# Kernel optimization log

Measured on AMD Instinct MI355X. Metric: run time of the kernel, lower is better.

## Reference

```python
import jax, jax.numpy as jnp
import numpy as np

B, C, N, T = 8, 32, 4000, 12
KT = 3
TS = 6          # tem_size
SUP_ORD_CH = (2 * 3 + 1) * C  # (order*support_len+1)*c_in = 224
EPS = 1e-5


def setup_inputs() -> dict:
    key = jax.random.key(0)
    ks = jax.random.split(key, 20)
    inp = {
        "x": jax.random.normal(ks[0], (B, C, N, T), dtype=jnp.float32),
        # dense normalized supports (scaled uniform, like row-normalized adjacency)
        "A0": jax.random.uniform(ks[1], (N, N), dtype=jnp.float32) / N,
        "A1": jax.random.uniform(ks[2], (N, N), dtype=jnp.float32) / N,
        "A2": jax.random.uniform(ks[3], (N, N), dtype=jnp.float32) / N,
        # conv1: 1x1 Conv2d(32 -> 32), bias
        "conv1_w": jax.random.normal(ks[4], (C, C), dtype=jnp.float32) * 0.05,
        "conv1_b": jnp.zeros((C,), dtype=jnp.float32),
        # multigcn mlp: Conv2d(224 -> 64, kernel (1, Kt)), bias
        "mlp_w": jax.random.normal(ks[5], (2 * C, SUP_ORD_CH, 1, KT), dtype=jnp.float32) * 0.02,
        "mlp_b": jnp.zeros((2 * C,), dtype=jnp.float32),
        # conv_temp1: 1x1 Conv2d over time axis (10 -> 6), bias
        "ct1_w": jax.random.normal(ks[6], (TS, T - KT + 1), dtype=jnp.float32) * 0.1,
        "ct1_b": jnp.zeros((TS,), dtype=jnp.float32),
        # TATT_1 params
        "tat_c1_w": jax.random.normal(ks[7], (C,), dtype=jnp.float32) * 0.1,   # Conv2d(c_in->1,1x1,no bias)
        "tat_c2_w": jax.random.normal(ks[8], (N,), dtype=jnp.float32) * 0.01,  # Conv2d(N->1,1x1,no bias)
        "tat_w": jax.random.normal(ks[9], (N, C), dtype=jnp.float32) * 0.01,
        "tat_bias": jnp.zeros((TS, TS), dtype=jnp.float32),
        "tat_v": jax.random.normal(ks[10], (TS, TS), dtype=jnp.float32) * 0.3,
        "bn1_g": jnp.ones((TS,), dtype=jnp.float32),
        "bn1_b": jnp.zeros((TS,), dtype=jnp.float32),
        # final BatchNorm2d(c_out)
        "bn2_g": jnp.ones((C,), dtype=jnp.float32),
        "bn2_b": jnp.zeros((C,), dtype=jnp.float32),
    }
    return inp


def reference(x, A0, A1, A2, conv1_w, conv1_b, mlp_w, mlp_b, ct1_w, ct1_b,
              tat_c1_w, tat_c2_w, tat_w, tat_bias, tat_v, bn1_g, bn1_b,
              bn2_g, bn2_b):
    # residual = conv1(x)  (1x1 conv over channels)
    residual = jnp.einsum('oc,bcnl->bonl', conv1_w, x) + conv1_b[None, :, None, None]

    # multi_gcn_time: nconv does A<-A.T then einsum('ncvl,vw->ncwl'),
    # i.e. out[..,w,..] = sum_v x[..,v,..] * A[w,v]
    outs = [x]
    for A in (A0, A1, A2):
        x1 = jnp.einsum('bcvl,wv->bcwl', x, A)
        outs.append(x1)
        x2 = jnp.einsum('bcvl,wv->bcwl', x1, A)
        outs.append(x2)
    h = jnp.concatenate(outs, axis=1)  # (B, 224, N, T)
    h = jax.lax.conv_general_dilated(
        h, mlp_w, window_strides=(1, 1), padding='VALID',
        dimension_numbers=('NCHW', 'OIHW', 'NCHW')) + mlp_b[None, :, None, None]  # (B,64,N,10)

    # gated tanh * sigmoid
    x1, x2 = jnp.split(h, 2, axis=1)
    g = jnp.tanh(x1) * jax.nn.sigmoid(x2)  # (B,32,N,10)

    # conv_temp1: 1x1 conv over the TIME axis (10 -> 6)
    g = jnp.einsum('ql,bcnl->bcnq', ct1_w, g) + ct1_b[None, None, None, :]  # (B,32,N,6)

    # TATT_1 temporal attention coefficients
    f1 = jnp.einsum('c,bcnt->btn', tat_c1_w, g)                       # (B,6,N)
    f2 = jnp.einsum('n,bcnt->bct', tat_c2_w, g)                       # (B,32,6)
    logits = jax.nn.sigmoid(jnp.einsum('btn,nc,bcs->bts', f1, tat_w, f2) + tat_bias)
    logits = jnp.einsum('ts,bsq->btq', tat_v, logits)                 # (B,6,6)
    # BatchNorm1d(tem_size) applied after permute(0,2,1): channel = q axis
    lp = jnp.transpose(logits, (0, 2, 1))
    mu = lp.mean(axis=(0, 2), keepdims=True)
    var = lp.var(axis=(0, 2), keepdims=True)
    lp = (lp - mu) / jnp.sqrt(var + EPS) * bn1_g[None, :, None] + bn1_b[None, :, None]
    logits = jnp.transpose(lp, (0, 2, 1))
    coefs = jax.nn.softmax(logits, axis=-1)                           # (B,6,6)

    # x = einsum('bcnl,blq->bcnq', x, T_coef.transpose(-1,-2))
    Tc = jnp.transpose(coefs, (0, 2, 1))
    out = jnp.einsum('bcnl,blq->bcnq', g, Tc)                         # (B,32,N,6)

    y = out + residual[:, :, :, -out.shape[3]:]
    # BatchNorm2d(c_out), training-mode batch stats
    mu2 = y.mean(axis=(0, 2, 3), keepdims=True)
    var2 = y.var(axis=(0, 2, 3), keepdims=True)
    return (y - mu2) / jnp.sqrt(var2 + EPS) * bn2_g[None, :, None, None] + bn2_b[None, :, None, None]
```

## Files before the change

### kernel.cpp

```cpp
#include <hip/hip_runtime.h>
#include <hip/hip_bf16.h>
#include <cstdint>
#include <cstddef>


typedef __attribute__((ext_vector_type(8))) short s16x8;
typedef __attribute__((ext_vector_type(4))) short s16x4;
typedef __attribute__((ext_vector_type(4))) float f32x4;

#define DEVFN __device__ __forceinline__

DEVFN void gload16(const void* g, void* l) {
  __builtin_amdgcn_global_load_lds((const __attribute__((address_space(1))) unsigned int*)g,
                                   (__attribute__((address_space(3))) unsigned int*)l, 16, 0, 0);
}

DEVFN unsigned short f2bf(float f) {
  union { float f; unsigned int u; } v; v.f = f;
  unsigned int u = v.u;
  return (unsigned short)((u + 0x7fffu + ((u >> 16) & 1u)) >> 16);
}

__global__ void k_transpose(const float* __restrict__ x,
                            unsigned short* __restrict__ Xt,
                            unsigned short* __restrict__ Scat) {
  __shared__ float ldsT[32 * 417];
  int v0 = blockIdx.x * 32;
  int b = blockIdx.y;
  int tid = threadIdx.x;
  for (int i = tid; i < 1024; i += 256) {
    int c = i >> 5, vv = i & 31;
    const float* src = x + ((size_t)(b * 32 + c) * 4000 + v0 + vv) * 12;
    f32x4 a0 = *(const f32x4*)(src);
    f32x4 a1 = *(const f32x4*)(src + 4);
    f32x4 a2 = *(const f32x4*)(src + 8);
    float* d = ldsT + c * 417 + vv * 13;
    d[0] = a0.x; d[1] = a0.y; d[2] = a0.z; d[3] = a0.w;
    d[4] = a1.x; d[5] = a1.y; d[6] = a1.z; d[7] = a1.w;
    d[8] = a2.x; d[9] = a2.y; d[10] = a2.z; d[11] = a2.w;
  }
  __syncthreads();
  for (int unit = tid; unit < 384; unit += 256) {
    int l = unit >> 5, c = unit & 31;
    alignas(16) unsigned short tmp[32];
#pragma unroll
    for (int vv = 0; vv < 32; ++vv) tmp[vv] = f2bf(ldsT[c * 417 + vv * 13 + l]);
    unsigned short* dst = Xt + (size_t)(b * 384 + l * 32 + c) * 4096 + v0;
#pragma unroll
    for (int j = 0; j < 4; ++j) *(s16x8*)(dst + j * 8) = *(const s16x8*)(tmp + j * 8);
  }
  for (int unit = tid; unit < 384; unit += 256) {
    int l = unit >> 5, vv = unit & 31;
    alignas(16) unsigned short tmp[32];
#pragma unroll
    for (int c = 0; c < 32; ++c) tmp[c] = f2bf(ldsT[c * 417 + vv * 13 + l]);
    int bn = b * 4000 + v0 + vv;
    unsigned short* dst = Scat + ((((size_t)l * 500 + (bn >> 6)) * 28) * 64 + (bn & 63)) * 8;
#pragma unroll
    for (int j = 0; j < 4; ++j) *(s16x8*)(dst + j * 512) = *(const s16x8*)(tmp + j * 8);
  }
}

__global__ void k_castA(const float* __restrict__ A, unsigned short* __restrict__ Abf) {
  int idx = blockIdx.x * 256 + threadIdx.x;
  int r = idx >> 10;
  int c4 = (idx & 1023) << 2;
  alignas(8) unsigned short o[4] = {0, 0, 0, 0};
  if (r < 4000 && c4 < 4000) {
    f32x4 v = *(const f32x4*)(A + (size_t)r * 4000 + c4);
    o[0] = f2bf(v.x); o[1] = f2bf(v.y); o[2] = f2bf(v.z); o[3] = f2bf(v.w);
  }
  *(s16x4*)(Abf + (size_t)r * 4096 + c4) = *(const s16x4*)o;
}

__global__ void k_wcat(const float* __restrict__ mlp_w, unsigned short* __restrict__ Wcat) {
  int i = blockIdx.x * 256 + threadIdx.x;
  if (i >= 43008) return;
  int e = i & 7;
  int j = (i >> 3) % 21;
  int rs = (i >> 3) / 21;
  int s = rs & 1, row = rs >> 1;
  int kt = j / 7, ks = j % 7;
  int p2 = row >> 6, g = (row >> 4) & 3, lr = row & 15;
  int oc = (s ? 32 : 0) + p2 * 16 + lr;
  int ic = ks * 32 + g * 8 + e;
  Wcat[i] = f2bf(mlp_w[((size_t)oc * 224 + ic) * 3 + kt]);
}

#define MFMA_(a, b, c) __builtin_amdgcn_mfma_f32_16x16x32_bf16(a, b, c, 0, 0, 0)

#define STGA3(ab, t) do {                                                        \
    const unsigned short* _s = aSrc + (size_t)(t) * 64;                          \
    unsigned short* _l = smem + (ab) * 12288;                                    \
    gload16(_s,          _l + tid * 8);                                          \
    gload16(_s + 262144, _l + (512 + tid) * 8);                                  \
    gload16(_s + 524288, _l + (1024 + tid) * 8);                                 \
  } while (0)

#define STGB3(pr, h, t) do {                                                     \
    const unsigned short* _s = bSrc + (size_t)(h) * 524288 + (size_t)(t) * 64;   \
    unsigned short* _l = smem + 36864 + ((pr) * 2 + (h)) * 8192;                 \
    gload16(_s,          _l + tid * 8);                                          \
    gload16(_s + 262144, _l + (512 + tid) * 8);                                  \
  } while (0)

#define LDA3(ab, f, kk) (*(const s16x8*)(smem + (ab) * 12288 + aoff + (f) * 1024 + ((kk) ? sxor : 0)))
#define LDB3(pr, nf, kk) (*(const s16x8*)(smem + 36864 + ((pr) * 2 + hb) * 8192 + boff + (nf) * 1024 + ((kk) ? sxor : 0)))

#define PHASE3(ab, pr, mp, FIRST, STAGE_CODE, VM) do {                           \
    s16x8 a00 = LDA3(ab, 2 * (mp), 0),     a01 = LDA3(ab, 2 * (mp), 1);          \
    s16x8 a10 = LDA3(ab, 2 * (mp) + 1, 0), a11 = LDA3(ab, 2 * (mp) + 1, 1);      \
    if (FIRST) {                                                                 \
      _Pragma("unroll")                                                          \
      for (int nf = 0; nf < 4; ++nf) { bfr[nf][0] = LDB3(pr, nf, 0); bfr[nf][1] = LDB3(pr, nf, 1); } \
    }                                                                            \
    STAGE_CODE;                                                                  \
    if ((VM) == 1)      asm volatile("s_waitcnt vmcnt(5)" ::: "memory");         \
    else if ((VM) == 2) asm volatile("s_waitcnt vmcnt(0)" ::: "memory");         \
    __builtin_amdgcn_s_barrier();                                                \
    asm volatile("s_waitcnt lgkmcnt(0)" ::: "memory");                           \
    __builtin_amdgcn_s_setprio(1);                                               \
    _Pragma("unroll")                                                            \
    for (int nf = 0; nf < 4; ++nf) {                                             \
      acc[2 * (mp)][nf]     = MFMA_(a00, bfr[nf][0], acc[2 * (mp)][nf]);         \
      acc[2 * (mp)][nf]     = MFMA_(a01, bfr[nf][1], acc[2 * (mp)][nf]);         \
      acc[2 * (mp) + 1][nf] = MFMA_(a10, bfr[nf][0], acc[2 * (mp) + 1][nf]);     \
      acc[2 * (mp) + 1][nf] = MFMA_(a11, bfr[nf][1], acc[2 * (mp) + 1][nf]);     \
    }                                                                            \
    __builtin_amdgcn_s_setprio(0);                                               \
  } while (0)

#define TILE3(A0, BT, S0, S1, S2, VM2) do {                                      \
    PHASE3(A0, BT, 0, 1, S0, 0);                                                 \
    PHASE3(A0, BT, 1, 0, S1, 0);                                                 \
    PHASE3(A0, BT, 2, 0, S2, VM2);                                               \
  } while (0)

template <int WRITE_C1>
__global__ __launch_bounds__(512, 2)
void k_gemm(const unsigned short* __restrict__ P, const unsigned short* __restrict__ Q,
            unsigned short* __restrict__ C1, unsigned short* __restrict__ Scat, int jslot) {
  extern __shared__ unsigned short smem[];
  int tid = threadIdx.x;
  int w = tid >> 6, lane = tid & 63;
  int lr = lane & 15, g = lane >> 4;
  int mq = w >> 2, nq = w & 3;
  int bid = blockIdx.x;
  int xcd = bid & 7, lid = bid >> 3;
  int nt = xcd * 2 + (lid >> 4);
  int mt = lid & 15;
  int m0 = mt * 192, n0 = nt * 256;
  int hb = nq >> 1;
  int slot0 = (g ^ (lr & 7)) * 8;
  int sxor = (slot0 & 32) ? -32 : 32;
  int aoff = (mq * 96 + lr) * 64 + slot0;
  int boff = ((nq & 1) * 64 + lr) * 64 + slot0;
  int gk = ((tid & 7) ^ ((tid >> 3) & 7)) * 8;
  const unsigned short* aSrc = P + (size_t)(m0 + (tid >> 3)) * 4096 + gk;
  const unsigned short* bSrc = Q + (size_t)(n0 + (tid >> 3)) * 4096 + gk;
  f32x4 acc[6][4] = {};
  s16x8 bfr[4][2];

  STGA3(0, 0);
  STGB3(0, 0, 0);
  STGB3(0, 1, 0);
  STGA3(1, 1);
  STGB3(1, 0, 1);
  asm volatile("s_waitcnt vmcnt(5)" ::: "memory");
  __builtin_amdgcn_s_barrier();

#pragma unroll 1
  for (int tb = 0; tb < 60; tb += 6) {
    TILE3(0, 0, STGB3(1, 1, tb + 1), STGA3(2, tb + 2), STGB3(0, 0, tb + 2), 1);
    TILE3(1, 1, STGB3(0, 1, tb + 2), STGA3(0, tb + 3), STGB3(1, 0, tb + 3), 1);
    TILE3(2, 0, STGB3(1, 1, tb + 3), STGA3(1, tb + 4), STGB3(0, 0, tb + 4), 1);
    TILE3(0, 1, STGB3(0, 1, tb + 4), STGA3(2, tb + 5), STGB3(1, 0, tb + 5), 1);
    TILE3(1, 0, STGB3(1, 1, tb + 5), STGA3(0, tb + 6), STGB3(0, 0, tb + 6), 1);
    TILE3(2, 1, STGB3(0, 1, tb + 6), STGA3(1, tb + 7), STGB3(1, 0, tb + 7), 1);
  }
  TILE3(0, 0, STGB3(1, 1, 61), STGA3(2, 62), STGB3(0, 0, 62), 1);
  TILE3(1, 1, STGB3(0, 1, 62), STGA3(0, 63), STGB3(1, 0, 63), 1);
  TILE3(2, 0, STGB3(1, 1, 63), (void)0,      (void)0,          2);
  TILE3(0, 1, (void)0,         (void)0,      (void)0,          0);

  asm volatile("s_waitcnt vmcnt(0) lgkmcnt(0)" ::: "memory");
  __syncthreads();
  unsigned short* eld = smem;
  int rb = g * 4;
#pragma unroll
  for (int f = 0; f < 6; ++f)
#pragma unroll
    for (int nf = 0; nf < 4; ++nf)
#pragma unroll
      for (int r = 0; r < 4; ++r)
        eld[(mq * 96 + f * 16 + rb + r) * 264 + nq * 64 + nf * 16 + lr] = f2bf(acc[f][nf][r]);
  __syncthreads();
  if (WRITE_C1) {
#pragma unroll
    for (int uu = 0; uu < 2; ++uu) {
      int u = uu * 512 + tid;
      if (u < 768) {
        int row = u >> 2, q = u & 3;
        unsigned short* dst = C1 + (size_t)(m0 + row) * 4096 + n0 + q * 64;
        const unsigned short* sp = eld + row * 264 + q * 64;
#pragma unroll
        for (int j = 0; j < 8; ++j) *(s16x8*)(dst + j * 8) = *(const s16x8*)(sp + j * 8);
      }
    }
  }
  int bb2 = m0 / 384, lb = (m0 % 384) >> 5;
#pragma unroll
  for (int uu = 0; uu < 3; ++uu) {
    int u = uu * 512 + tid;
    int lg = u >> 8, nl = u & 255;
    int node = n0 + nl;
    if (node < 4000) {
      alignas(16) unsigned short tmp[32];
#pragma unroll
      for (int c = 0; c < 32; ++c) tmp[c] = eld[(lg * 32 + c) * 264 + nl];
      int bn = bb2 * 4000 + node;
      int l2 = lb + lg;
      unsigned short* d2 = Scat + ((((size_t)l2 * 500 + (bn >> 6)) * 28 + jslot) * 64 + (bn & 63)) * 8;
#pragma unroll
      for (int j = 0; j < 4; ++j) *(s16x8*)(d2 + j * 512) = *(const s16x8*)(tmp + j * 8);
    }
  }
}

#define MLPSTG(L, BUF) do {                                                    \
    const unsigned short* _sb = Scat + ((size_t)(L) * 500 + grp) * 14336;      \
    unsigned short* _lb = lds + (BUF) * 14336;                                 \
    gload16(_sb + tid * 8,          _lb + tid * 8);                            \
    gload16(_sb + (512 + tid) * 8,  _lb + (512 + tid) * 8);                    \
    gload16(_sb + (1024 + tid) * 8, _lb + (1024 + tid) * 8);                   \
    if (tid < 256) gload16(_sb + (1536 + tid) * 8, _lb + (1536 + tid) * 8);    \
  } while (0)

__global__ __launch_bounds__(512, 2)
void k_mlp(const unsigned short* __restrict__ Wcat, const unsigned short* __restrict__ Scat,
           const float* __restrict__ mlp_b, const float* __restrict__ ct1_w,
           const float* __restrict__ ct1_b, float* __restrict__ g6) {
  __shared__ unsigned short lds[2 * 14336];
  int tid = threadIdx.x;
  int grp = blockIdx.x;
  int w = tid >> 6, lane = tid & 63;
  int lr = lane & 15, g = lane >> 4;
  int p2 = w & 1, bnq = w >> 1;
  const unsigned short* wrow = Wcat + (size_t)(((p2 * 4 + g) * 16 + lr) * 2) * 168;
  s16x8 wa[21], wb[21];
#pragma unroll
  for (int j = 0; j < 21; ++j) {
    wa[j] = *(const s16x8*)(wrow + j * 8);
    wb[j] = *(const s16x8*)(wrow + 168 + j * 8);
  }
  float mb1[4], mb2[4];
#pragma unroll
  for (int r = 0; r < 4; ++r) {
    mb1[r] = mlp_b[p2 * 16 + g * 4 + r];
    mb2[r] = mlp_b[32 + p2 * 16 + g * 4 + r];
  }
  f32x4 acc[3][2];
  float g6a[4][6] = {};

  MLPSTG(0, 0);
  asm volatile("s_waitcnt vmcnt(0)" ::: "memory");
  __syncthreads();

#pragma unroll
  for (int l = 0; l < 12; ++l) {
    if (l < 11) MLPSTG(l + 1, (l + 1) & 1);
    if (l <= 9) {
      acc[l % 3][0] = (f32x4){0.f, 0.f, 0.f, 0.f};
      acc[l % 3][1] = (f32x4){0.f, 0.f, 0.f, 0.f};
    }
    const unsigned short* sb = lds + (l & 1) * 14336;
#pragma unroll
    for (int kt = 0; kt < 3; ++kt) {
      int t = l - kt;
      if (t < 0 || t > 9) continue;
      int st = t % 3;
#pragma unroll
      for (int ks = 0; ks < 7; ++ks) {
        int j = kt * 7 + ks;
        s16x8 bb = *(const s16x8*)(sb + ((ks * 4 + g) * 64 + bnq * 16 + lr) * 8);
        acc[st][0] = MFMA_(wa[j], bb, acc[st][0]);
        acc[st][1] = MFMA_(wb[j], bb, acc[st][1]);
      }
    }
    if (l >= 2) {
      int t = l - 2, st = t % 3;
#pragma unroll
      for (int r = 0; r < 4; ++r) {
        float v1 = acc[st][0][r] + mb1[r];
        float v2 = acc[st][1][r] + mb2[r];
        float gg = tanhf(v1) * (1.0f / (1.0f + __expf(-v2)));
#pragma unroll
        for (int q6 = 0; q6 < 6; ++q6) g6a[r][q6] += ct1_w[q6 * 10 + t] * gg;
      }
    }
    asm volatile("s_waitcnt vmcnt(0)" ::: "memory");
    __syncthreads();
  }

  int nglob = grp * 64 + bnq * 16 + lr;
  int b = nglob / 4000, nn = nglob - b * 4000;
#pragma unroll
  for (int r = 0; r < 4; ++r) {
    int c = p2 * 16 + g * 4 + r;
    float* op = g6 + ((size_t)(b * 32 + c) * 4000 + nn) * 6;
#pragma unroll
    for (int q6 = 0; q6 < 6; ++q6) op[q6] = g6a[r][q6] + ct1_b[q6];
  }
}

__global__ void k_f1(const float* __restrict__ g6, const float* __restrict__ c1,
                     float* __restrict__ f1) {
  int idx = blockIdx.x * 128 + threadIdx.x;
  if (idx >= 8 * 4000) return;
  int n = idx % 4000, b = idx / 4000;
  float acc[6] = {};
  const float* gp = g6 + ((size_t)b * 32 * 4000 + n) * 6;
  for (int c = 0; c < 32; ++c) {
    float wv = c1[c];
    const float* p = gp + (size_t)c * 4000 * 6;
#pragma unroll
    for (int t = 0; t < 6; ++t) acc[t] += wv * p[t];
  }
  for (int t = 0; t < 6; ++t) f1[((size_t)b * 6 + t) * 4000 + n] = acc[t];
}

__global__ void k_f2(const float* __restrict__ g6, const float* __restrict__ c2,
                     float* __restrict__ f2) {
  __shared__ float red[256 * 6];
  int bc = blockIdx.x;
  int tid = threadIdx.x;
  float acc[6] = {};
  const float* gp = g6 + (size_t)bc * 4000 * 6;
  for (int n = tid; n < 4000; n += 256) {
    float wv = c2[n];
#pragma unroll
    for (int t = 0; t < 6; ++t) acc[t] += wv * gp[(size_t)n * 6 + t];
  }
  for (int t = 0; t < 6; ++t) red[tid * 6 + t] = acc[t];
  __syncthreads();
  for (int s = 128; s > 0; s >>= 1) {
    if (tid < s)
      for (int t = 0; t < 6; ++t) red[tid * 6 + t] += red[(tid + s) * 6 + t];
    __syncthreads();
  }
  if (tid < 6) f2[bc * 6 + tid] = red[tid];
}

__global__ void k_m1(const float* __restrict__ f1, const float* __restrict__ tw,
                     float* __restrict__ m1) {
  __shared__ float red[8][32];
  int bt = blockIdx.x;
  int nc = blockIdx.y;
  int tid = threadIdx.x;
  int c = tid & 31, gi = tid >> 5;
  float acc = 0.f;
  const float* fp = f1 + (size_t)bt * 4000 + nc * 250;
  const float* twp = tw + ((size_t)nc * 250) * 32 + c;
  for (int n = gi; n < 250; n += 8) acc += fp[n] * twp[n * 32];
  red[gi][c] = acc;
  __syncthreads();
  if (tid < 32) {
    float s = 0.f;
#pragma unroll
    for (int gg = 0; gg < 8; ++gg) s += red[gg][c];
    atomicAdd(&m1[(size_t)bt * 32 + c], s);
  }
}

__global__ void k_att(const float* __restrict__ m1, const float* __restrict__ f2,
                      const float* __restrict__ bias, const float* __restrict__ tv,
                      const float* __restrict__ g1, const float* __restrict__ b1,
                      float* __restrict__ coefs) {
  __shared__ float sig[48 * 6], lgs[48 * 6], mu[6], iv[6];
  int tid = threadIdx.x;
  int b = tid / 6, t = tid % 6;
  if (tid < 48) {
    for (int s = 0; s < 6; ++s) {
      float a = bias[t * 6 + s];
      for (int c = 0; c < 32; ++c)
        a += m1[((size_t)b * 6 + t) * 32 + c] * f2[((size_t)b * 32 + c) * 6 + s];
      sig[tid * 6 + s] = 1.0f / (1.0f + __expf(-a));
    }
  }
  __syncthreads();
  if (tid < 48) {
    for (int q = 0; q < 6; ++q) {
      float a = 0.f;
      for (int s = 0; s < 6; ++s) a += tv[t * 6 + s] * sig[(b * 6 + s) * 6 + q];
      lgs[tid * 6 + q] = a;
    }
  }
  __syncthreads();
  if (tid < 6) {
    float s = 0, s2 = 0;
    for (int r = 0; r < 48; ++r) { float v = lgs[r * 6 + tid]; s += v; s2 += v * v; }
    float m = s / 48.f;
    mu[tid] = m;
    iv[tid] = rsqrtf(s2 / 48.f - m * m + 1e-5f);
  }
  __syncthreads();
  if (tid < 48) {
    float v[6], mx = -1e30f;
    for (int q = 0; q < 6; ++q) {
      v[q] = (lgs[tid * 6 + q] - mu[q]) * iv[q] * g1[q] + b1[q];
      mx = fmaxf(mx, v[q]);
    }
    float s = 0;
    for (int q = 0; q < 6; ++q) { v[q] = __expf(v[q] - mx); s += v[q]; }
    float inv = 1.0f / s;
    for (int q = 0; q < 6; ++q) coefs[tid * 6 + q] = v[q] * inv;
  }
}

__global__ void k_final1(const float* __restrict__ x, const float* __restrict__ cw,
                         const float* __restrict__ cb, const float* __restrict__ g6,
                         const float* __restrict__ coefs, float* __restrict__ out) {
  __shared__ float xt[32 * 8 * 6];
  __shared__ float cwT[1024];
  __shared__ float cfs[36], cbs[32];
  int n0 = blockIdx.x * 8;
  int b = blockIdx.y;
  int tid = threadIdx.x;
  {
    int ci = tid >> 3, seg = tid & 7;
    const float* xp = x + ((size_t)(b * 32 + ci) * 4000 + n0 + seg) * 12 + 6;
#pragma unroll
    for (int q = 0; q < 6; ++q) xt[(ci * 8 + seg) * 6 + q] = xp[q];
  }
  for (int i = tid; i < 1024; i += 256) { int o = i >> 5, ci = i & 31; cwT[ci * 32 + o] = cw[i]; }
  if (tid < 36) cfs[tid] = coefs[b * 36 + tid];
  if (tid < 32) cbs[tid] = cb[tid];
  __syncthreads();
  int nn = tid & 7, c = tid >> 3;
  const float* gp = g6 + ((size_t)(b * 32 + c) * 4000 + n0 + nn) * 6;
  float gv[6];
#pragma unroll
  for (int l = 0; l < 6; ++l) gv[l] = gp[l];
  float y[6];
#pragma unroll
  for (int q = 0; q < 6; ++q) {
    float at = 0.f;
#pragma unroll
    for (int l = 0; l < 6; ++l) at += gv[l] * cfs[q * 6 + l];
    y[q] = at + cbs[c];
  }
  for (int ci = 0; ci < 32; ++ci) {
    float wv = cwT[ci * 32 + c];
#pragma unroll
    for (int q = 0; q < 6; ++q) y[q] += wv * xt[(ci * 8 + nn) * 6 + q];
  }
  float* op = out + ((size_t)(b * 32 + c) * 4000 + n0 + nn) * 6;
#pragma unroll
  for (int q = 0; q < 6; ++q) op[q] = y[q];
}

__global__ void k_stats(const float* __restrict__ out, float* __restrict__ stats) {
  __shared__ float r1[4], r2[4];
  int bc = blockIdx.y;
  int c = bc & 31;
  int tid = threadIdx.x;
  const float* p = out + (size_t)bc * 24000 + blockIdx.x * 6000;
  float s = 0.f, s2 = 0.f;
  for (int i = tid * 4; i < 6000; i += 1024) {
    f32x4 v = *(const f32x4*)(p + i);
    s  += v.x + v.y + v.z + v.w;
    s2 += v.x * v.x + v.y * v.y + v.z * v.z + v.w * v.w;
  }
#pragma unroll
  for (int off = 32; off > 0; off >>= 1) {
    s  += __shfl_down(s, off);
    s2 += __shfl_down(s2, off);
  }
  int lane = tid & 63, w = tid >> 6;
  if (lane == 0) { r1[w] = s; r2[w] = s2; }
  __syncthreads();
  if (tid == 0) {
    atomicAdd(&stats[c],      r1[0] + r1[1] + r1[2] + r1[3]);
    atomicAdd(&stats[32 + c], r2[0] + r2[1] + r2[2] + r2[3]);
  }
}

__global__ void k_final2(float* __restrict__ out, const float* __restrict__ stats,
                         const float* __restrict__ g2, const float* __restrict__ b2) {
  int idx = (blockIdx.x * 256 + threadIdx.x) * 4;
  if (idx >= 6144000) return;
  int c = (idx / 24000) % 32;
  float mean = stats[c] * (1.0f / 192000.f);
  float var = stats[32 + c] * (1.0f / 192000.f) - mean * mean;
  float sc = rsqrtf(var + 1e-5f) * g2[c];
  float sh = b2[c] - mean * sc;
  f32x4 v = *(f32x4*)(out + idx);
  v.x = v.x * sc + sh; v.y = v.y * sc + sh; v.z = v.z * sc + sh; v.w = v.w * sc + sh;
  *(f32x4*)(out + idx) = v;
}

extern "C" void kernel_launch(void* const* d_in, const int* in_sizes, int n_in,
                              void* d_out, int out_size, void* d_ws, size_t ws_size,
                              hipStream_t stream) {
  (void)in_sizes; (void)n_in; (void)out_size;
  const float* x       = (const float*)d_in[0];
  const float* A[3]    = {(const float*)d_in[1], (const float*)d_in[2], (const float*)d_in[3]};
  const float* conv1_w = (const float*)d_in[4];
  const float* conv1_b = (const float*)d_in[5];
  const float* mlp_w   = (const float*)d_in[6];
  const float* mlp_b   = (const float*)d_in[7];
  const float* ct1_w   = (const float*)d_in[8];
  const float* ct1_b   = (const float*)d_in[9];
  const float* c1w     = (const float*)d_in[10];
  const float* c2w     = (const float*)d_in[11];
  const float* tw      = (const float*)d_in[12];
  const float* tbias   = (const float*)d_in[13];
  const float* tv      = (const float*)d_in[14];
  const float* bn1g    = (const float*)d_in[15];
  const float* bn1b    = (const float*)d_in[16];
  const float* bn2g    = (const float*)d_in[17];
  const float* bn2b    = (const float*)d_in[18];
  float* out = (float*)d_out;

  char* ws = (char*)d_ws;
  size_t off = 0;
  auto alloc = [&](size_t bytes) { size_t r = off; off += (bytes + 255) & ~(size_t)255; return r; };
  size_t oScat = alloc(172032000);
  size_t oXt   = alloc(25165824);
  size_t oA    = alloc(33554432);
  size_t oY1t  = alloc(25165824);
  size_t oWcat = alloc(86016);
  size_t oF1 = alloc(768000);
  size_t oF2 = alloc(6144);
  size_t oM1 = alloc(6144);
  size_t oCf = alloc(1152);
  size_t oSt = alloc(256);
  if (ws_size < off) return;

  unsigned short* Scat = (unsigned short*)(ws + oScat);
  unsigned short* Xt   = (unsigned short*)(ws + oXt);
  float*          g6   = (float*)(ws + oXt);
  unsigned short* Abf  = (unsigned short*)(ws + oA);
  unsigned short* Y1t  = (unsigned short*)(ws + oY1t);
  unsigned short* Wcat = (unsigned short*)(ws + oWcat);

  hipFuncSetAttribute((const void*)k_gemm<0>, hipFuncAttributeMaxDynamicSharedMemorySize, 139264);
  hipFuncSetAttribute((const void*)k_gemm<1>, hipFuncAttributeMaxDynamicSharedMemorySize, 139264);

  hipMemsetAsync(Xt, 0, 25165824, stream);
  hipMemsetAsync(ws + oSt, 0, 256, stream);
  hipMemsetAsync(ws + oM1, 0, 6144, stream);
  k_transpose<<<dim3(125, 8), 256, 0, stream>>>(x, Xt, Scat);
  k_wcat<<<168, 256, 0, stream>>>(mlp_w, Wcat);
  for (int i = 0; i < 3; ++i) {
    k_castA<<<16384, 256, 0, stream>>>(A[i], Abf);
    k_gemm<1><<<256, 512, 139264, stream>>>(Xt, Abf, Y1t, Scat, (2 * i + 1) * 4);
    k_gemm<0><<<256, 512, 139264, stream>>>(Y1t, Abf, nullptr, Scat, (2 * i + 2) * 4);
  }
  k_mlp<<<500, 512, 0, stream>>>(Wcat, Scat, mlp_b, ct1_w, ct1_b, g6);
  k_f1<<<250, 128, 0, stream>>>(g6, c1w, (float*)(ws + oF1));
  k_f2<<<256, 256, 0, stream>>>(g6, c2w, (float*)(ws + oF2));
  k_m1<<<dim3(48, 16), 256, 0, stream>>>((float*)(ws + oF1), tw, (float*)(ws + oM1));
  k_att<<<1, 64, 0, stream>>>((float*)(ws + oM1), (float*)(ws + oF2), tbias, tv, bn1g, bn1b,
                              (float*)(ws + oCf));
  k_final1<<<dim3(500, 8), 256, 0, stream>>>(x, conv1_w, conv1_b, g6, (float*)(ws + oCf), out);
  k_stats<<<dim3(4, 256), 256, 0, stream>>>(out, (float*)(ws + oSt));
  k_final2<<<6000, 256, 0, stream>>>(out, (float*)(ws + oSt), bn2g, bn2b);
}
```

Baseline: 739.8 us.

## Triple-buffer k_mlp LDS staging and store g6 in time-major layout

```diff
diff --git a/kernel.cpp b/kernel.cpp
--- a/kernel.cpp
+++ b/kernel.cpp
@@ -236,11 +236,11 @@
     if (tid < 256) gload16(_sb + (1536 + tid) * 8, _lb + (1536 + tid) * 8);    \
   } while (0)
 
-__global__ __launch_bounds__(512, 2)
+__global__ __launch_bounds__(512, 1)
 void k_mlp(const unsigned short* __restrict__ Wcat, const unsigned short* __restrict__ Scat,
            const float* __restrict__ mlp_b, const float* __restrict__ ct1_w,
            const float* __restrict__ ct1_b, float* __restrict__ g6) {
-  __shared__ unsigned short lds[2 * 14336];
+  extern __shared__ unsigned short lds[];
   int tid = threadIdx.x;
   int grp = blockIdx.x;
   int w = tid >> 6, lane = tid & 63;
@@ -263,17 +263,18 @@
   float g6a[4][6] = {};
 
   MLPSTG(0, 0);
-  asm volatile("s_waitcnt vmcnt(0)" ::: "memory");
+  MLPSTG(1, 1);
+  asm volatile("s_waitcnt vmcnt(3)" ::: "memory");
   __syncthreads();
 
 #pragma unroll
   for (int l = 0; l < 12; ++l) {
-    if (l < 11) MLPSTG(l + 1, (l + 1) & 1);
+    if (l <= 9) MLPSTG(l + 2, (l + 2) % 3);
     if (l <= 9) {
       acc[l % 3][0] = (f32x4){0.f, 0.f, 0.f, 0.f};
       acc[l % 3][1] = (f32x4){0.f, 0.f, 0.f, 0.f};
     }
-    const unsigned short* sb = lds + (l & 1) * 14336;
+    const unsigned short* sb = lds + (l % 3) * 14336;
 #pragma unroll
     for (int kt = 0; kt < 3; ++kt) {
       int t = l - kt;
@@ -298,8 +299,9 @@
         for (int q6 = 0; q6 < 6; ++q6) g6a[r][q6] += ct1_w[q6 * 10 + t] * gg;
       }
     }
-    asm volatile("s_waitcnt vmcnt(0)" ::: "memory");
-    __syncthreads();
+    if (l <= 9)       asm volatile("s_waitcnt vmcnt(3)" ::: "memory");
+    else if (l == 10) asm volatile("s_waitcnt vmcnt(0)" ::: "memory");
+    if (l < 11) __syncthreads();
   }
 
   int nglob = grp * 64 + bnq * 16 + lr;
@@ -307,9 +309,9 @@
 #pragma unroll
   for (int r = 0; r < 4; ++r) {
     int c = p2 * 16 + g * 4 + r;
-    float* op = g6 + ((size_t)(b * 32 + c) * 4000 + nn) * 6;
-#pragma unroll
-    for (int q6 = 0; q6 < 6; ++q6) op[q6] = g6a[r][q6] + ct1_b[q6];
+#pragma unroll
+    for (int q6 = 0; q6 < 6; ++q6)
+      g6[((size_t)(b * 6 + q6) * 32 + c) * 4000 + nn] = g6a[r][q6] + ct1_b[q6];
   }
 }
 
@@ -319,12 +321,11 @@
   if (idx >= 8 * 4000) return;
   int n = idx % 4000, b = idx / 4000;
   float acc[6] = {};
-  const float* gp = g6 + ((size_t)b * 32 * 4000 + n) * 6;
   for (int c = 0; c < 32; ++c) {
     float wv = c1[c];
-    const float* p = gp + (size_t)c * 4000 * 6;
-#pragma unroll
-    for (int t = 0; t < 6; ++t) acc[t] += wv * p[t];
+#pragma unroll
+    for (int t = 0; t < 6; ++t)
+      acc[t] += wv * g6[((size_t)(b * 6 + t) * 32 + c) * 4000 + n];
   }
   for (int t = 0; t < 6; ++t) f1[((size_t)b * 6 + t) * 4000 + n] = acc[t];
 }
@@ -333,13 +334,14 @@
                      float* __restrict__ f2) {
   __shared__ float red[256 * 6];
   int bc = blockIdx.x;
+  int b = bc >> 5, c = bc & 31;
   int tid = threadIdx.x;
   float acc[6] = {};
-  const float* gp = g6 + (size_t)bc * 4000 * 6;
   for (int n = tid; n < 4000; n += 256) {
     float wv = c2[n];
 #pragma unroll
-    for (int t = 0; t < 6; ++t) acc[t] += wv * gp[(size_t)n * 6 + t];
+    for (int t = 0; t < 6; ++t)
+      acc[t] += wv * g6[((size_t)(b * 6 + t) * 32 + c) * 4000 + n];
   }
   for (int t = 0; t < 6; ++t) red[tid * 6 + t] = acc[t];
   __syncthreads();
@@ -437,10 +439,10 @@
   if (tid < 32) cbs[tid] = cb[tid];
   __syncthreads();
   int nn = tid & 7, c = tid >> 3;
-  const float* gp = g6 + ((size_t)(b * 32 + c) * 4000 + n0 + nn) * 6;
   float gv[6];
 #pragma unroll
-  for (int l = 0; l < 6; ++l) gv[l] = gp[l];
+  for (int l = 0; l < 6; ++l)
+    gv[l] = g6[((size_t)(b * 6 + l) * 32 + c) * 4000 + n0 + nn];
   float y[6];
 #pragma unroll
   for (int q = 0; q < 6; ++q) {
@@ -546,6 +548,7 @@
 
   hipFuncSetAttribute((const void*)k_gemm<0>, hipFuncAttributeMaxDynamicSharedMemorySize, 139264);
   hipFuncSetAttribute((const void*)k_gemm<1>, hipFuncAttributeMaxDynamicSharedMemorySize, 139264);
+  hipFuncSetAttribute((const void*)k_mlp, hipFuncAttributeMaxDynamicSharedMemorySize, 86016);
 
   hipMemsetAsync(Xt, 0, 25165824, stream);
   hipMemsetAsync(ws + oSt, 0, 256, stream);
@@ -557,7 +560,7 @@
     k_gemm<1><<<256, 512, 139264, stream>>>(Xt, Abf, Y1t, Scat, (2 * i + 1) * 4);
     k_gemm<0><<<256, 512, 139264, stream>>>(Y1t, Abf, nullptr, Scat, (2 * i + 2) * 4);
   }
-  k_mlp<<<500, 512, 0, stream>>>(Wcat, Scat, mlp_b, ct1_w, ct1_b, g6);
+  k_mlp<<<500, 512, 86016, stream>>>(Wcat, Scat, mlp_b, ct1_w, ct1_b, g6);
   k_f1<<<250, 128, 0, stream>>>(g6, c1w, (float*)(ws + oF1));
   k_f2<<<256, 256, 0, stream>>>(g6, c2w, (float*)(ws + oF2));
   k_m1<<<dim3(48, 16), 256, 0, stream>>>((float*)(ws + oF1), tw, (float*)(ws + oM1));
```

Measured after the change: 748.3 us. About the same (+1.1%).

## Store g6 in time-major channel-innermost layout with coalesced writes and reads

Applied to the files above, without the earlier changes.

```diff
diff --git a/kernel.cpp b/kernel.cpp
--- a/kernel.cpp
+++ b/kernel.cpp
@@ -302,53 +302,61 @@
     __syncthreads();
   }
 
-  int nglob = grp * 64 + bnq * 16 + lr;
-  int b = nglob / 4000, nn = nglob - b * 4000;
-#pragma unroll
-  for (int r = 0; r < 4; ++r) {
-    int c = p2 * 16 + g * 4 + r;
-    float* op = g6 + ((size_t)(b * 32 + c) * 4000 + nn) * 6;
-#pragma unroll
-    for (int q6 = 0; q6 < 6; ++q6) op[q6] = g6a[r][q6] + ct1_b[q6];
+  float* lout = (float*)lds;
+  int nnl = bnq * 16 + lr;
+  int cbase = p2 * 16 + g * 4;
+#pragma unroll
+  for (int q6 = 0; q6 < 6; ++q6)
+#pragma unroll
+    for (int r = 0; r < 4; ++r)
+      lout[(q6 * 64 + nnl) * 32 + cbase + r] = g6a[r][q6] + ct1_b[q6];
+  __syncthreads();
+  int base = grp * 64;
+#pragma unroll
+  for (int it = 0; it < 6; ++it) {
+    int i = it * 512 + tid;
+    int q = i >> 9, rem = i & 511;
+    *(f32x4*)(g6 + ((size_t)q * 32000 + base) * 32 + rem * 4) =
+        *(const f32x4*)(lout + q * 2048 + rem * 4);
   }
 }
 
 __global__ void k_f1(const float* __restrict__ g6, const float* __restrict__ c1,
                      float* __restrict__ f1) {
-  int idx = blockIdx.x * 128 + threadIdx.x;
-  if (idx >= 8 * 4000) return;
-  int n = idx % 4000, b = idx / 4000;
-  float acc[6] = {};
-  const float* gp = g6 + ((size_t)b * 32 * 4000 + n) * 6;
-  for (int c = 0; c < 32; ++c) {
-    float wv = c1[c];
-    const float* p = gp + (size_t)c * 4000 * 6;
-#pragma unroll
-    for (int t = 0; t < 6; ++t) acc[t] += wv * p[t];
-  }
-  for (int t = 0; t < 6; ++t) f1[((size_t)b * 6 + t) * 4000 + n] = acc[t];
+  int nb = blockIdx.x * 8 + (threadIdx.x >> 5);
+  int c = threadIdx.x & 31;
+  if (nb >= 32000) return;
+  int b = nb / 4000, n = nb - b * 4000;
+  float wv = c1[c];
+#pragma unroll
+  for (int t = 0; t < 6; ++t) {
+    float v = wv * g6[((size_t)t * 32000 + nb) * 32 + c];
+#pragma unroll
+    for (int off = 16; off > 0; off >>= 1) v += __shfl_down(v, off, 32);
+    if (c == 0) f1[((size_t)b * 6 + t) * 4000 + n] = v;
+  }
 }
 
 __global__ void k_f2(const float* __restrict__ g6, const float* __restrict__ c2,
                      float* __restrict__ f2) {
-  __shared__ float red[256 * 6];
-  int bc = blockIdx.x;
-  int tid = threadIdx.x;
-  float acc[6] = {};
-  const float* gp = g6 + (size_t)bc * 4000 * 6;
-  for (int n = tid; n < 4000; n += 256) {
-    float wv = c2[n];
-#pragma unroll
-    for (int t = 0; t < 6; ++t) acc[t] += wv * gp[(size_t)n * 6 + t];
-  }
-  for (int t = 0; t < 6; ++t) red[tid * 6 + t] = acc[t];
-  __syncthreads();
-  for (int s = 128; s > 0; s >>= 1) {
-    if (tid < s)
-      for (int t = 0; t < 6; ++t) red[tid * 6 + t] += red[(tid + s) * 6 + t];
-    __syncthreads();
-  }
-  if (tid < 6) f2[bc * 6 + tid] = red[tid];
+  __shared__ float red[8][32];
+  int bt = blockIdx.x;
+  int b = bt / 6, t = bt % 6;
+  int nc = blockIdx.y;
+  int tid = threadIdx.x;
+  int c = tid & 31, ng = tid >> 5;
+  float a = 0.f;
+  const float* gp = g6 + ((size_t)t * 32000 + b * 4000 + nc * 250) * 32;
+  const float* cp = c2 + nc * 250;
+  for (int n = ng; n < 250; n += 8) a += cp[n] * gp[(size_t)n * 32 + c];
+  red[ng][c] = a;
+  __syncthreads();
+  if (tid < 32) {
+    float s = 0.f;
+#pragma unroll
+    for (int gg = 0; gg < 8; ++gg) s += red[gg][c];
+    atomicAdd(&f2[((size_t)b * 32 + c) * 6 + t], s);
+  }
 }
 
 __global__ void k_m1(const float* __restrict__ f1, const float* __restrict__ tw,
@@ -421,6 +429,7 @@
                          const float* __restrict__ cb, const float* __restrict__ g6,
                          const float* __restrict__ coefs, float* __restrict__ out) {
   __shared__ float xt[32 * 8 * 6];
+  __shared__ float gslab[6 * 8 * 32];
   __shared__ float cwT[1024];
   __shared__ float cfs[36], cbs[32];
   int n0 = blockIdx.x * 8;
@@ -432,15 +441,19 @@
 #pragma unroll
     for (int q = 0; q < 6; ++q) xt[(ci * 8 + seg) * 6 + q] = xp[q];
   }
+#pragma unroll
+  for (int i = tid; i < 1536; i += 256) {
+    int l = i >> 8, rem = i & 255;
+    gslab[i] = g6[((size_t)l * 32000 + b * 4000 + n0) * 32 + rem];
+  }
   for (int i = tid; i < 1024; i += 256) { int o = i >> 5, ci = i & 31; cwT[ci * 32 + o] = cw[i]; }
   if (tid < 36) cfs[tid] = coefs[b * 36 + tid];
   if (tid < 32) cbs[tid] = cb[tid];
   __syncthreads();
   int nn = tid & 7, c = tid >> 3;
-  const float* gp = g6 + ((size_t)(b * 32 + c) * 4000 + n0 + nn) * 6;
   float gv[6];
 #pragma unroll
-  for (int l = 0; l < 6; ++l) gv[l] = gp[l];
+  for (int l = 0; l < 6; ++l) gv[l] = gslab[l * 256 + nn * 32 + c];
   float y[6];
 #pragma unroll
   for (int q = 0; q < 6; ++q) {
@@ -550,6 +563,7 @@
   hipMemsetAsync(Xt, 0, 25165824, stream);
   hipMemsetAsync(ws + oSt, 0, 256, stream);
   hipMemsetAsync(ws + oM1, 0, 6144, stream);
+  hipMemsetAsync(ws + oF2, 0, 6144, stream);
   k_transpose<<<dim3(125, 8), 256, 0, stream>>>(x, Xt, Scat);
   k_wcat<<<168, 256, 0, stream>>>(mlp_w, Wcat);
   for (int i = 0; i < 3; ++i) {
@@ -558,8 +572,8 @@
     k_gemm<0><<<256, 512, 139264, stream>>>(Y1t, Abf, nullptr, Scat, (2 * i + 2) * 4);
   }
   k_mlp<<<500, 512, 0, stream>>>(Wcat, Scat, mlp_b, ct1_w, ct1_b, g6);
-  k_f1<<<250, 128, 0, stream>>>(g6, c1w, (float*)(ws + oF1));
-  k_f2<<<256, 256, 0, stream>>>(g6, c2w, (float*)(ws + oF2));
+  k_f1<<<4000, 256, 0, stream>>>(g6, c1w, (float*)(ws + oF1));
+  k_f2<<<dim3(48, 16), 256, 0, stream>>>(g6, c2w, (float*)(ws + oF2));
   k_m1<<<dim3(48, 16), 256, 0, stream>>>((float*)(ws + oF1), tw, (float*)(ws + oM1));
   k_att<<<1, 64, 0, stream>>>((float*)(ws + oM1), (float*)(ws + oF2), tbias, tv, bn1g, bn1b,
                               (float*)(ws + oCf));
```

Result: no change. 747.2 us (+1.0%).
